# Kernel optimization log

Measured on AMD Instinct MI355X. Metric: run time of the kernel, lower is better.

Reference implementation:

```python
import jax, jax.numpy as jnp
import numpy as np

B, S, D = 4, 2048, 1024
H, DK, DV = 16, 64, 64

def setup_inputs() -> dict:
    key = jax.random.key(0)
    ks = jax.random.split(key, 8)
    def xavier(k, fan_in, fan_out):
        limit = float(np.sqrt(6.0 / (fan_in + fan_out)))
        return jax.random.uniform(k, (fan_in, fan_out), jnp.float32, -limit, limit)
    return {
        "Q": jax.random.normal(ks[0], (B, S, D), jnp.float32),
        "K": jax.random.normal(ks[1], (B, S, D), jnp.float32),
        "V": jax.random.normal(ks[2], (B, S, D), jnp.float32),
        "mask": jax.random.uniform(ks[3], (B, S), jnp.float32),
        "Wq": xavier(ks[4], D, H * DK),  # stored [in, out]; torch Linear applies x @ W.T
        "bq": jnp.zeros((H * DK,), jnp.float32),
        "Wk": xavier(ks[5], D, H * DK),
        "bk": jnp.zeros((H * DK,), jnp.float32),
        "Wv": xavier(ks[6], D, H * DV),
        "bv": jnp.zeros((H * DV,), jnp.float32),
    }

def reference(Q, K, V, mask, Wq, bq, Wk, bk, Wv, bv):
    b, s, _ = Q.shape
    # projections -> [b, h, s, d]
    q = (Q @ Wq + bq).reshape(b, s, H, DK).transpose(0, 2, 1, 3)
    k = (K @ Wk + bk).reshape(b, s, H, DK).transpose(0, 2, 1, 3)
    v = (V @ Wv + bv).reshape(b, s, H, DV).transpose(0, 2, 1, 3)
    scores = jnp.einsum('bhqd,bhkd->bhqk', q, k) / jnp.sqrt(jnp.float32(DK))
    e = jnp.exp(scores)  # NOTE: raw exp, no max-subtraction (faithful to source)
    e = e * mask[:, None, None, :]  # multiplicative mask over key dim
    attn = e / (jnp.sum(e, axis=-1, keepdims=True) + 1e-8)
    context = jnp.einsum('bhqk,bhkd->bhqd', attn, v)
    return context.transpose(0, 2, 1, 3).reshape(b, s, H * DV)
```

## Files before the change

### kernel.cpp

```cpp
#include <hip/hip_runtime.h>
#include <hip/hip_bf16.h>
#include <stdint.h>

typedef short bf16x8 __attribute__((ext_vector_type(8)));
typedef float f32x4 __attribute__((ext_vector_type(4)));
typedef unsigned int u32x2 __attribute__((ext_vector_type(2)));
typedef unsigned int u32x4 __attribute__((ext_vector_type(4)));

__device__ __forceinline__ unsigned short f2bf(float f) {
  union { float f; unsigned u; } x; x.f = f;
  unsigned r = x.u + 0x7FFFu + ((x.u >> 16) & 1u);
  return (unsigned short)(r >> 16);
}

__device__ __forceinline__ unsigned pk2bf(float a, float b) {
  union { __hip_bfloat162 h; unsigned u; } x;
  x.h = __float22bfloat162_rn(make_float2(a, b));
  return x.u;
}

typedef const __attribute__((address_space(1))) unsigned int* gptr_t;
typedef __attribute__((address_space(3))) unsigned int* lptr_t;
__device__ __forceinline__ void gll16(const void* g, void* l) {
  __builtin_amdgcn_global_load_lds((gptr_t)g, (lptr_t)l, 16, 0, 0);
}

__global__ __launch_bounds__(1024) void wt_kernel(const float* __restrict__ Wq,
                                                  const float* __restrict__ Wk,
                                                  const float* __restrict__ Wv,
                                                  unsigned short* __restrict__ wt) {
  const float* W = blockIdx.z == 0 ? Wq : (blockIdx.z == 1 ? Wk : Wv);
  unsigned short* o = wt + (size_t)blockIdx.z * 1048576;
  __shared__ float t[32][33];
  int tx = threadIdx.x, ty = threadIdx.y;
  t[ty][tx] = W[(size_t)(blockIdx.y * 32 + ty) * 1024 + blockIdx.x * 32 + tx];
  __syncthreads();
  o[(size_t)(blockIdx.x * 32 + ty) * 1024 + blockIdx.y * 32 + tx] = f2bf(t[tx][ty]);
}

__global__ __launch_bounds__(256) void cvt_kernel(const float* __restrict__ Q,
                                                  const float* __restrict__ K,
                                                  const float* __restrict__ V,
                                                  unsigned short* __restrict__ out) {
  int y = blockIdx.y;
  const float* s = y == 0 ? Q : (y == 1 ? K : V);
  unsigned short* o = out + (size_t)y * 8388608;
  size_t idx = ((size_t)blockIdx.x * 256 + threadIdx.x) * 8;
  float4 f0 = *(const float4*)(s + idx);
  float4 f1 = *(const float4*)(s + idx + 4);
  u32x4 r = {pk2bf(f0.x, f0.y), pk2bf(f0.z, f0.w), pk2bf(f1.x, f1.y), pk2bf(f1.z, f1.w)};
  *(u32x4*)(o + idx) = r;
}

__global__ __launch_bounds__(256) void proj_kernel(
    const unsigned short* __restrict__ Xb, const unsigned short* __restrict__ wt,
    const float* __restrict__ bq, const float* __restrict__ bk, const float* __restrict__ bv,
    unsigned short* __restrict__ qo, unsigned short* __restrict__ ko, unsigned short* __restrict__ vo) {
  int p = blockIdx.z;
  const unsigned short* X = Xb + (size_t)p * 8388608;
  const unsigned short* Wt = wt + (size_t)p * 1048576;
  const float* bias = p == 0 ? bq : (p == 1 ? bk : bv);
  unsigned short* out = p == 0 ? qo : (p == 1 ? ko : vo);

  __shared__ __align__(16) unsigned short abuf[8192];
  __shared__ __align__(16) unsigned short bbuf[8192];

  int tid = threadIdx.x;
  int lane = tid & 63, w = tid >> 6;
  int l15 = lane & 15, quad = lane >> 4;
  int wm = w >> 1, wn = w & 1;
  int m0 = blockIdx.x * 128, n0 = blockIdx.y * 128;

  f32x4 acc[4][4] = {};

  for (int kk = 0; kk < 16; ++kk) {
    int k0 = kk * 64;
    for (int j = 0; j < 4; ++j) {
      int stj = w * 4 + j;
      int kt = stj >> 3, t = stj & 7;
      gll16(Wt + (size_t)(n0 + t * 16 + l15) * 1024 + k0 + kt * 32 + quad * 8, &bbuf[stj * 512]);
      gll16(X + (size_t)(m0 + t * 16 + l15) * 1024 + k0 + kt * 32 + quad * 8, &abuf[stj * 512]);
    }
    __syncthreads();
    for (int kt = 0; kt < 2; ++kt) {
      bf16x8 af[4], bfr[4];
      for (int i = 0; i < 4; ++i) af[i]  = *(const bf16x8*)&abuf[(kt * 8 + wm * 4 + i) * 512 + lane * 8];
      for (int j = 0; j < 4; ++j) bfr[j] = *(const bf16x8*)&bbuf[(kt * 8 + wn * 4 + j) * 512 + lane * 8];
      for (int i = 0; i < 4; ++i)
        for (int j = 0; j < 4; ++j)
          acc[i][j] = __builtin_amdgcn_mfma_f32_16x16x32_bf16(af[i], bfr[j], acc[i][j], 0, 0, 0);
    }
    __syncthreads();
  }

  bool isv = (p == 2);
  for (int j = 0; j < 4; ++j) {
    int n = n0 + wn * 64 + j * 16 + l15;
    float bl = bias[n];
    int h = n >> 6, d = n & 63;
    for (int i = 0; i < 4; ++i) {
      for (int r = 0; r < 4; ++r) {
        int m = m0 + wm * 64 + i * 16 + quad * 4 + r;
        int b = m >> 11, s = m & 2047;
        float val = acc[i][j][r] + bl;
        size_t idx;
        if (isv) idx = ((size_t)((b * 16 + h) * 64 + d) << 11) + s;
        else     idx = ((size_t)((b * 16 + h) * 2048 + s) << 6) + d;
        out[idx] = f2bf(val);
      }
    }
  }
}

__global__ __launch_bounds__(256, 3) void attn_kernel(
    const unsigned short* __restrict__ q, const unsigned short* __restrict__ k,
    const unsigned short* __restrict__ vT, const float* __restrict__ mask,
    float* __restrict__ out) {
  int qb = blockIdx.x, h = blockIdx.y, b = blockIdx.z;
  int tid = threadIdx.x, lane = tid & 63, w = tid >> 6;
  int l15 = lane & 15, quad = lane >> 4;

  __shared__ __align__(16) unsigned short un[16384];
  __shared__ __align__(16) unsigned short vls[8192];

  const unsigned short* qp = q + (size_t)(b * 16 + h) * 2048 * 64;
  const unsigned short* kp = k + (size_t)(b * 16 + h) * 2048 * 64;
  const unsigned short* vp = vT + (size_t)(b * 16 + h) * 64 * 2048;
  const float* mp = mask + (size_t)b * 2048;

  bf16x8 aq[2][2];
  for (int nt = 0; nt < 2; ++nt)
    for (int kt = 0; kt < 2; ++kt)
      aq[nt][kt] = *(const bf16x8*)(qp + (size_t)(qb * 128 + w * 32 + nt * 16 + l15) * 64 + kt * 32 + quad * 8);

  f32x4 oacc[2][4] = {};
  f32x4 dacc[2] = {};
  bf16x8 ones = {0x3F80, 0x3F80, 0x3F80, 0x3F80, 0x3F80, 0x3F80, 0x3F80, 0x3F80};

  unsigned short* pw = &un[w * 4096];

  for (int kb = 0; kb < 16; ++kb) {
    int kbase = kb * 128;
    for (int j = 0; j < 4; ++j) {
      int stj = w * 4 + j;
      int kt = stj >> 3, t = stj & 7;
      gll16(kp + (size_t)(kbase + t * 16 + l15) * 64 + kt * 32 + quad * 8, &un[stj * 512]);
      int kt2 = stj >> 2, t2 = stj & 3;
      gll16(vp + (size_t)(t2 * 16 + l15) * 2048 + kbase + kt2 * 32 + quad * 8, &vls[stj * 512]);
    }
    __syncthreads();

    f32x4 sacc[8][2] = {};
    for (int mt16 = 0; mt16 < 8; ++mt16)
      for (int kt = 0; kt < 2; ++kt) {
        bf16x8 ak = *(const bf16x8*)&un[(kt * 8 + mt16) * 512 + lane * 8];
        sacc[mt16][0] = __builtin_amdgcn_mfma_f32_16x16x32_bf16(ak, aq[0][kt], sacc[mt16][0], 0, 0, 0);
        sacc[mt16][1] = __builtin_amdgcn_mfma_f32_16x16x32_bf16(ak, aq[1][kt], sacc[mt16][1], 0, 0, 0);
      }

    __syncthreads();

    for (int mt16 = 0; mt16 < 8; ++mt16) {
      float4 mv = *(const float4*)&mp[kbase + mt16 * 16 + quad * 4];
      const float* mm = (const float*)&mv;
      for (int nt = 0; nt < 2; ++nt) {
        float e0 = __expf(sacc[mt16][nt][0] * 0.125f) * mm[0];
        float e1 = __expf(sacc[mt16][nt][1] * 0.125f) * mm[1];
        float e2 = __expf(sacc[mt16][nt][2] * 0.125f) * mm[2];
        float e3 = __expf(sacc[mt16][nt][3] * 0.125f) * mm[3];
        u32x2 wv = {pk2bf(e0, e1), pk2bf(e2, e3)};
        *(u32x2*)&pw[(nt * 8 + mt16) * 256 + lane * 4] = wv;
      }
    }

    for (int kt = 0; kt < 4; ++kt) {
      int t = kt * 2 + (quad >> 1);
      int srcl = ((quad & 1) * 2) * 16 + l15;
      bf16x8 pa[2];
      for (int mt = 0; mt < 2; ++mt) {
        union { u32x2 p[2]; bf16x8 v; } u;
        int base = (mt * 8 + t) * 256 + srcl * 4;
        u.p[0] = *(const u32x2*)&pw[base];
        u.p[1] = *(const u32x2*)&pw[base + 64];
        pa[mt] = u.v;
      }
      dacc[0] = __builtin_amdgcn_mfma_f32_16x16x32_bf16(pa[0], ones, dacc[0], 0, 0, 0);
      dacc[1] = __builtin_amdgcn_mfma_f32_16x16x32_bf16(pa[1], ones, dacc[1], 0, 0, 0);
      for (int nt = 0; nt < 4; ++nt) {
        bf16x8 bv = *(const bf16x8*)&vls[(kt * 4 + nt) * 512 + lane * 8];
        oacc[0][nt] = __builtin_amdgcn_mfma_f32_16x16x32_bf16(pa[0], bv, oacc[0][nt], 0, 0, 0);
        oacc[1][nt] = __builtin_amdgcn_mfma_f32_16x16x32_bf16(pa[1], bv, oacc[1][nt], 0, 0, 0);
      }
    }
    __syncthreads();
  }

  for (int mt = 0; mt < 2; ++mt)
    for (int r = 0; r < 4; ++r) {
      int s = qb * 128 + w * 32 + mt * 16 + quad * 4 + r;
      float rden = 1.0f / (dacc[mt][r] + 1e-8f);
      for (int nt = 0; nt < 4; ++nt) {
        int dv = nt * 16 + l15;
        out[(size_t)(b * 2048 + s) * 1024 + h * 64 + dv] = oacc[mt][nt][r] * rden;
      }
    }
}

extern "C" void kernel_launch(void* const* d_in, const int* in_sizes, int n_in,
                              void* d_out, int out_size, void* d_ws, size_t ws_size,
                              hipStream_t stream) {
  const float* Q    = (const float*)d_in[0];
  const float* K    = (const float*)d_in[1];
  const float* V    = (const float*)d_in[2];
  const float* mask = (const float*)d_in[3];
  const float* Wq   = (const float*)d_in[4];
  const float* bq   = (const float*)d_in[5];
  const float* Wk   = (const float*)d_in[6];
  const float* bk   = (const float*)d_in[7];
  const float* Wv   = (const float*)d_in[8];
  const float* bv   = (const float*)d_in[9];

  char* ws = (char*)d_ws;
  unsigned short* wt = (unsigned short*)ws;
  unsigned short* qb = (unsigned short*)(ws + 6291456);
  unsigned short* kb = (unsigned short*)(ws + 23068672);
  unsigned short* vb = (unsigned short*)(ws + 39845888);
  unsigned short* xb = (unsigned short*)(ws + 56623104);

  hipLaunchKernelGGL(wt_kernel, dim3(32, 32, 3), dim3(32, 32), 0, stream, Wq, Wk, Wv, wt);
  hipLaunchKernelGGL(cvt_kernel, dim3(4096, 3), dim3(256), 0, stream, Q, K, V, xb);
  hipLaunchKernelGGL(proj_kernel, dim3(64, 8, 3), dim3(256), 0, stream,
                     xb, wt, bq, bk, bv, qb, kb, vb);
  hipLaunchKernelGGL(attn_kernel, dim3(16, 16, 4), dim3(256), 0, stream,
                     qb, kb, vb, mask, (float*)d_out);
}
```

Baseline: 436.8 us.

## Double-buffer K/V tiles and use 8 waves per attention block

The attention kernel now runs 512 threads (8 waves, 16 query rows each) instead of 4 waves of 32 rows. K/V tiles shrink to 64 keys and are double-buffered in LDS, so the next tile is prefetched during compute and one barrier per iteration is dropped. The goal is to hide global-to-LDS latency and raise occupancy, at the cost of less Q-fragment reuse per K/V load and more loop iterations.

```diff
diff --git a/kernel.cpp b/kernel.cpp
--- a/kernel.cpp
+++ b/kernel.cpp
@@ -112,7 +112,7 @@
   }
 }
 
-__global__ __launch_bounds__(256, 3) void attn_kernel(
+__global__ __launch_bounds__(512, 6) void attn_kernel(
     const unsigned short* __restrict__ q, const unsigned short* __restrict__ k,
     const unsigned short* __restrict__ vT, const float* __restrict__ mask,
     float* __restrict__ out) {
@@ -120,90 +120,86 @@
   int tid = threadIdx.x, lane = tid & 63, w = tid >> 6;
   int l15 = lane & 15, quad = lane >> 4;
 
-  __shared__ __align__(16) unsigned short un[16384];
-  __shared__ __align__(16) unsigned short vls[8192];
+  __shared__ __align__(16) unsigned short kbuf[2][4096];
+  __shared__ __align__(16) unsigned short vbuf[2][4096];
+  __shared__ __align__(16) unsigned short pbuf[8][1024];
 
   const unsigned short* qp = q + (size_t)(b * 16 + h) * 2048 * 64;
   const unsigned short* kp = k + (size_t)(b * 16 + h) * 2048 * 64;
   const unsigned short* vp = vT + (size_t)(b * 16 + h) * 64 * 2048;
   const float* mp = mask + (size_t)b * 2048;
 
-  bf16x8 aq[2][2];
-  for (int nt = 0; nt < 2; ++nt)
-    for (int kt = 0; kt < 2; ++kt)
-      aq[nt][kt] = *(const bf16x8*)(qp + (size_t)(qb * 128 + w * 32 + nt * 16 + l15) * 64 + kt * 32 + quad * 8);
-
-  f32x4 oacc[2][4] = {};
-  f32x4 dacc[2] = {};
+  bf16x8 aq[2];
+  for (int kt = 0; kt < 2; ++kt)
+    aq[kt] = *(const bf16x8*)(qp + (size_t)(qb * 128 + w * 16 + l15) * 64 + kt * 32 + quad * 8);
+
+  f32x4 oacc[4] = {};
+  f32x4 dacc = {};
   bf16x8 ones = {0x3F80, 0x3F80, 0x3F80, 0x3F80, 0x3F80, 0x3F80, 0x3F80, 0x3F80};
 
-  unsigned short* pw = &un[w * 4096];
-
-  for (int kb = 0; kb < 16; ++kb) {
-    int kbase = kb * 128;
-    for (int j = 0; j < 4; ++j) {
-      int stj = w * 4 + j;
-      int kt = stj >> 3, t = stj & 7;
-      gll16(kp + (size_t)(kbase + t * 16 + l15) * 64 + kt * 32 + quad * 8, &un[stj * 512]);
-      int kt2 = stj >> 2, t2 = stj & 3;
-      gll16(vp + (size_t)(t2 * 16 + l15) * 2048 + kbase + kt2 * 32 + quad * 8, &vls[stj * 512]);
+  unsigned short* pw = pbuf[w];
+
+  int skt = w >> 2, sm = w & 3;
+  const unsigned short* ksrc0 = kp + (size_t)(sm * 16 + l15) * 64 + skt * 32 + quad * 8;
+  const unsigned short* vsrc0 = vp + (size_t)(sm * 16 + l15) * 2048 + skt * 32 + quad * 8;
+
+#define STAGE(bi, t)                                    \
+  do {                                                  \
+    gll16(ksrc0 + (size_t)(t) * 64 * 64, &kbuf[bi][w * 512]); \
+    gll16(vsrc0 + (size_t)(t) * 64,      &vbuf[bi][w * 512]); \
+  } while (0)
+
+  STAGE(0, 0);
+  __syncthreads();
+
+  for (int t = 0; t < 32; ++t) {
+    int cur = t & 1;
+    if (t + 1 < 32) STAGE(cur ^ 1, t + 1);
+
+    f32x4 sacc[4] = {};
+    for (int m = 0; m < 4; ++m)
+      for (int kt = 0; kt < 2; ++kt) {
+        bf16x8 ak = *(const bf16x8*)&kbuf[cur][(kt * 4 + m) * 512 + lane * 8];
+        sacc[m] = __builtin_amdgcn_mfma_f32_16x16x32_bf16(ak, aq[kt], sacc[m], 0, 0, 0);
+      }
+
+    int kbase = t * 64;
+    for (int m = 0; m < 4; ++m) {
+      float4 mv = *(const float4*)&mp[kbase + m * 16 + quad * 4];
+      const float* mm = (const float*)&mv;
+      float e0 = __expf(sacc[m][0] * 0.125f) * mm[0];
+      float e1 = __expf(sacc[m][1] * 0.125f) * mm[1];
+      float e2 = __expf(sacc[m][2] * 0.125f) * mm[2];
+      float e3 = __expf(sacc[m][3] * 0.125f) * mm[3];
+      u32x2 wv = {pk2bf(e0, e1), pk2bf(e2, e3)};
+      *(u32x2*)&pw[m * 256 + lane * 4] = wv;
+    }
+
+    for (int kt = 0; kt < 2; ++kt) {
+      int tt = kt * 2 + (quad >> 1);
+      int srcl = (quad & 1) * 32 + l15;
+      union { u32x2 p[2]; bf16x8 v; } u;
+      u.p[0] = *(const u32x2*)&pw[tt * 256 + srcl * 4];
+      u.p[1] = *(const u32x2*)&pw[tt * 256 + srcl * 4 + 64];
+      bf16x8 pa = u.v;
+      dacc = __builtin_amdgcn_mfma_f32_16x16x32_bf16(pa, ones, dacc, 0, 0, 0);
+      for (int nt = 0; nt < 4; ++nt) {
+        bf16x8 bv = *(const bf16x8*)&vbuf[cur][(kt * 4 + nt) * 512 + lane * 8];
+        oacc[nt] = __builtin_amdgcn_mfma_f32_16x16x32_bf16(pa, bv, oacc[nt], 0, 0, 0);
+      }
     }
     __syncthreads();
-
-    f32x4 sacc[8][2] = {};
-    for (int mt16 = 0; mt16 < 8; ++mt16)
-      for (int kt = 0; kt < 2; ++kt) {
-        bf16x8 ak = *(const bf16x8*)&un[(kt * 8 + mt16) * 512 + lane * 8];
-        sacc[mt16][0] = __builtin_amdgcn_mfma_f32_16x16x32_bf16(ak, aq[0][kt], sacc[mt16][0], 0, 0, 0);
-        sacc[mt16][1] = __builtin_amdgcn_mfma_f32_16x16x32_bf16(ak, aq[1][kt], sacc[mt16][1], 0, 0, 0);
-      }
-
-    __syncthreads();
-
-    for (int mt16 = 0; mt16 < 8; ++mt16) {
-      float4 mv = *(const float4*)&mp[kbase + mt16 * 16 + quad * 4];
-      const float* mm = (const float*)&mv;
-      for (int nt = 0; nt < 2; ++nt) {
-        float e0 = __expf(sacc[mt16][nt][0] * 0.125f) * mm[0];
-        float e1 = __expf(sacc[mt16][nt][1] * 0.125f) * mm[1];
-        float e2 = __expf(sacc[mt16][nt][2] * 0.125f) * mm[2];
-        float e3 = __expf(sacc[mt16][nt][3] * 0.125f) * mm[3];
-        u32x2 wv = {pk2bf(e0, e1), pk2bf(e2, e3)};
-        *(u32x2*)&pw[(nt * 8 + mt16) * 256 + lane * 4] = wv;
-      }
-    }
-
-    for (int kt = 0; kt < 4; ++kt) {
-      int t = kt * 2 + (quad >> 1);
-      int srcl = ((quad & 1) * 2) * 16 + l15;
-      bf16x8 pa[2];
-      for (int mt = 0; mt < 2; ++mt) {
-        union { u32x2 p[2]; bf16x8 v; } u;
-        int base = (mt * 8 + t) * 256 + srcl * 4;
-        u.p[0] = *(const u32x2*)&pw[base];
-        u.p[1] = *(const u32x2*)&pw[base + 64];
-        pa[mt] = u.v;
-      }
-      dacc[0] = __builtin_amdgcn_mfma_f32_16x16x32_bf16(pa[0], ones, dacc[0], 0, 0, 0);
-      dacc[1] = __builtin_amdgcn_mfma_f32_16x16x32_bf16(pa[1], ones, dacc[1], 0, 0, 0);
-      for (int nt = 0; nt < 4; ++nt) {
-        bf16x8 bv = *(const bf16x8*)&vls[(kt * 4 + nt) * 512 + lane * 8];
-        oacc[0][nt] = __builtin_amdgcn_mfma_f32_16x16x32_bf16(pa[0], bv, oacc[0][nt], 0, 0, 0);
-        oacc[1][nt] = __builtin_amdgcn_mfma_f32_16x16x32_bf16(pa[1], bv, oacc[1][nt], 0, 0, 0);
-      }
-    }
-    __syncthreads();
-  }
-
-  for (int mt = 0; mt < 2; ++mt)
-    for (int r = 0; r < 4; ++r) {
-      int s = qb * 128 + w * 32 + mt * 16 + quad * 4 + r;
-      float rden = 1.0f / (dacc[mt][r] + 1e-8f);
-      for (int nt = 0; nt < 4; ++nt) {
-        int dv = nt * 16 + l15;
-        out[(size_t)(b * 2048 + s) * 1024 + h * 64 + dv] = oacc[mt][nt][r] * rden;
-      }
-    }
+  }
+#undef STAGE
+
+  for (int r = 0; r < 4; ++r) {
+    int s = qb * 128 + w * 16 + quad * 4 + r;
+    float rden = 1.0f / (dacc[r] + 1e-8f);
+    for (int nt = 0; nt < 4; ++nt) {
+      int dv = nt * 16 + l15;
+      out[(size_t)(b * 2048 + s) * 1024 + h * 64 + dv] = oacc[nt][r] * rden;
+    }
+  }
 }
 
 extern "C" void kernel_launch(void* const* d_in, const int* in_sizes, int n_in,
@@ -231,6 +227,6 @@
   hipLaunchKernelGGL(cvt_kernel, dim3(4096, 3), dim3(256), 0, stream, Q, K, V, xb);
   hipLaunchKernelGGL(proj_kernel, dim3(64, 8, 3), dim3(256), 0, stream,
                      xb, wt, bq, bk, bv, qb, kb, vb);
-  hipLaunchKernelGGL(attn_kernel, dim3(16, 16, 4), dim3(256), 0, stream,
+  hipLaunchKernelGGL(attn_kernel, dim3(16, 16, 4), dim3(512), 0, stream,
                      qb, kb, vb, mask, (float*)d_out);
 }
```

Result: faster. 418.8 us (-4.1%).
